# Kernel optimization log

Hardware: AMD Instinct MI355X
Metric: run time of the kernel (lower is better)

## Reference

```python
import jax, jax.numpy as jnp
import numpy as np

ADDR_BITS = 20      # AttentionMemory addr_bits
VAL_BITS = 32       # AttentionMemory value_bits
MAX_ENTRIES = 1024  # preallocated buffer size (torch default 4096, reduced)
TEMP = 10.0         # registered temperature buffer
B, T, R = 16, 128, 2048  # batch of memories, sequential writes, reads


def _encode(x, nbits):
    # BinaryEncoder: int -> +/-1 bit vector [..., nbits]
    bits = jnp.right_shift(x[..., None], jnp.arange(nbits, dtype=x.dtype)) & 1
    return bits.astype(jnp.float32) * 2.0 - 1.0


def setup_inputs() -> dict:
    key = jax.random.key(0)
    k1, k2, k3 = jax.random.split(key, 3)
    waddr = jax.random.randint(k1, (B, T), 0, 1 << ADDR_BITS, dtype=jnp.int32)
    wval = jax.random.randint(k2, (B, T), 0, 2**31 - 1, dtype=jnp.int32)
    raddr = jax.random.randint(k3, (B, R), 0, 1 << ADDR_BITS, dtype=jnp.int32)
    return {
        "write_addr_enc": _encode(waddr, ADDR_BITS),  # [B,T,20]
        "write_val_enc": _encode(wval, VAL_BITS),     # [B,T,32]
        "read_addr_enc": _encode(raddr, ADDR_BITS),   # [B,R,20]
    }


def reference(write_addr_enc, write_val_enc, read_addr_enc):
    E = MAX_ENTRIES
    ar = jnp.arange(E)
    keys0 = jnp.zeros((B, E, ADDR_BITS), jnp.float32)
    vals0 = jnp.zeros((B, E, VAL_BITS), jnp.float32)
    count0 = jnp.zeros((B,), jnp.int32)

    def step(state, inp):
        keys, values, count = state
        addr, val = inp  # [B,20], [B,32]
        scores = jnp.einsum('bea,ba->be', keys, addr)            # [B,E]
        valid = ar[None, :] < count[:, None]
        masked = jnp.where(valid, scores, -1e9)
        # torch: if max_score > addr_bits-1 -> overwrite argmax, else append
        overwrite = masked.max(axis=1) > (ADDR_BITS - 1)         # [B]
        idx = jnp.where(overwrite, jnp.argmax(masked, axis=1), count)
        onehot = ar[None, :] == idx[:, None]                     # [B,E]
        values = jnp.where(onehot[..., None], val[:, None, :], values)
        keys = jnp.where((onehot & ~overwrite[:, None])[..., None],
                         addr[:, None, :], keys)
        count = count + (~overwrite).astype(jnp.int32)
        return (keys, values, count), None

    (keys, values, count), _ = jax.lax.scan(
        step, (keys0, vals0, count0),
        (write_addr_enc.transpose(1, 0, 2), write_val_enc.transpose(1, 0, 2)))

    # AttentionMemory.read: softmax(keys @ addr * temperature) @ values
    rscores = jnp.einsum('bea,bra->bre', keys, read_addr_enc)    # [B,R,E]
    valid = ar[None, None, :] < count[:, None, None]
    rscores = jnp.where(valid, rscores * TEMP, -1e9)
    weights = jax.nn.softmax(rscores, axis=-1)
    return jnp.einsum('bre,bev->brv', weights, values)           # [B,R,32]
```

## Files before the change

kernel.cpp:

```cpp
#include <hip/hip_runtime.h>
#include <hip/hip_bf16.h>

#define B_DIM 16
#define T_DIM 128
#define R_DIM 2048
#define ABITS 20
#define VBITS 32
#define RPB   32
#define BLOCKS_PER_B (R_DIM / RPB)

__global__ __launch_bounds__(256) void fused_kernel(
    const float* __restrict__ waddr,
    const float* __restrict__ wval,
    const float* __restrict__ raddr,
    float* __restrict__ out)
{
    const int b    = blockIdx.x / BLOCKS_PER_B;
    const int rblk = blockIdx.x % BLOCKS_PER_B;
    const int t    = threadIdx.x;

    __shared__ unsigned s_addr[T_DIM];
    __shared__ unsigned s_val[T_DIM];
    __shared__ unsigned s_key[T_DIM];
    __shared__ unsigned s_vbits[T_DIM];
    __shared__ int      s_slotmap[T_DIM];
    __shared__ float    s_f[RPB * ABITS];
    __shared__ unsigned s_valT[VBITS * 4];
    __shared__ int      s_n;

    if (t == 0) s_n = 0;

    const float4* rp = (const float4*)(raddr + ((size_t)b * R_DIM + (size_t)rblk * RPB) * ABITS);
    if (t < RPB * ABITS / 4) ((float4*)s_f)[t] = rp[t];

    if (t < T_DIM) {
        const float4* ap = (const float4*)(waddr + (size_t)(b * T_DIM + t) * ABITS);
        unsigned a = 0;
        #pragma unroll
        for (int q = 0; q < ABITS / 4; ++q) {
            float4 f = ap[q];
            a |= (unsigned)(f.x > 0.f) << (4 * q + 0);
            a |= (unsigned)(f.y > 0.f) << (4 * q + 1);
            a |= (unsigned)(f.z > 0.f) << (4 * q + 2);
            a |= (unsigned)(f.w > 0.f) << (4 * q + 3);
        }
        s_addr[t] = a;
    } else {
        const int tv = t - T_DIM;
        const float4* vp = (const float4*)(wval + (size_t)(b * T_DIM + tv) * VBITS);
        unsigned v = 0;
        #pragma unroll
        for (int q = 0; q < VBITS / 4; ++q) {
            float4 f = vp[q];
            v |= (unsigned)(f.x > 0.f) << (4 * q + 0);
            v |= (unsigned)(f.y > 0.f) << (4 * q + 1);
            v |= (unsigned)(f.z > 0.f) << (4 * q + 2);
            v |= (unsigned)(f.w > 0.f) << (4 * q + 3);
        }
        s_val[tv] = v;
    }
    __syncthreads();

    int lastc = 0, t0 = t;
    if (t < T_DIM) {
        const unsigned a = s_addr[t];
        int firstc = 0;
        const uint4* a4 = (const uint4*)s_addr;
        #pragma unroll 8
        for (int u4 = 0; u4 < T_DIM / 4; ++u4) {
            uint4 kk = a4[u4];
            int u = u4 * 4;
            int e0 = (kk.x == a), e1 = (kk.y == a), e2 = (kk.z == a), e3 = (kk.w == a);
            firstc |= (e0 & (u + 0 < t)) | (e1 & (u + 1 < t)) | (e2 & (u + 2 < t)) | (e3 & (u + 3 < t));
            lastc  |= (e0 & (u + 0 > t)) | (e1 & (u + 1 > t)) | (e2 & (u + 2 > t)) | (e3 & (u + 3 > t));
            t0 = (e0 && (u + 0 < t0)) ? (u + 0) : t0;
            t0 = (e1 && (u + 1 < t0)) ? (u + 1) : t0;
            t0 = (e2 && (u + 2 < t0)) ? (u + 2) : t0;
            t0 = (e3 && (u + 3 < t0)) ? (u + 3) : t0;
        }
        if (!firstc) {
            int slot = atomicAdd(&s_n, 1);
            s_key[slot] = a;
            s_slotmap[t] = slot;
        }
    }
    __syncthreads();
    const int n = s_n;
    if (t < T_DIM && !lastc)
        s_vbits[s_slotmap[t0]] = s_val[t];
    __syncthreads();

    if (t < 128) {
        const int j = t & 31, w = t >> 5;
        unsigned word = 0;
        #pragma unroll 8
        for (int i = 0; i < 32; ++i)
            word |= ((s_vbits[w * 32 + i] >> j) & 1u) << i;
        s_valT[j * 4 + w] = word;
    }

    const int rl = t >> 3;
    const int k  = t & 7;
    const float* f = s_f + rl * ABITS;
    unsigned ra = 0;
    #pragma unroll
    for (int i = 0; i < ABITS; ++i) ra |= (unsigned)(f[i] > 0.f) << i;

    const uint4* k4 = (const uint4*)s_key;
    int dmin = 127;
    #pragma unroll
    for (int j = 0; j < 4; ++j) {
        uint4 kk = k4[k * 4 + j];
        int e = k * 16 + j * 4;
        int d0 = __popc(kk.x ^ ra) | ((e + 0 >= n) ? 64 : 0);
        int d1 = __popc(kk.y ^ ra) | ((e + 1 >= n) ? 64 : 0);
        int d2 = __popc(kk.z ^ ra) | ((e + 2 >= n) ? 64 : 0);
        int d3 = __popc(kk.w ^ ra) | ((e + 3 >= n) ? 64 : 0);
        dmin = min(dmin, min(min(d0, d1), min(d2, d3)));
    }
    dmin = min(dmin, __shfl_xor(dmin, 1, 8));
    dmin = min(dmin, __shfl_xor(dmin, 2, 8));
    dmin = min(dmin, __shfl_xor(dmin, 4, 8));

    unsigned mask = 0;
    #pragma unroll
    for (int j = 0; j < 4; ++j) {
        uint4 kk = k4[k * 4 + j];
        int e = k * 16 + j * 4;
        mask |= (unsigned)((__popc(kk.x ^ ra) | ((e + 0 >= n) ? 64 : 0)) == dmin) << (j * 4 + 0);
        mask |= (unsigned)((__popc(kk.y ^ ra) | ((e + 1 >= n) ? 64 : 0)) == dmin) << (j * 4 + 1);
        mask |= (unsigned)((__popc(kk.z ^ ra) | ((e + 2 >= n) ? 64 : 0)) == dmin) << (j * 4 + 2);
        mask |= (unsigned)((__popc(kk.w ^ ra) | ((e + 3 >= n) ? 64 : 0)) == dmin) << (j * 4 + 3);
    }

    unsigned m0 = (unsigned)__shfl((int)mask, 0, 8) | ((unsigned)__shfl((int)mask, 1, 8) << 16);
    unsigned m1 = (unsigned)__shfl((int)mask, 2, 8) | ((unsigned)__shfl((int)mask, 3, 8) << 16);
    unsigned m2 = (unsigned)__shfl((int)mask, 4, 8) | ((unsigned)__shfl((int)mask, 5, 8) << 16);
    unsigned m3 = (unsigned)__shfl((int)mask, 6, 8) | ((unsigned)__shfl((int)mask, 7, 8) << 16);

    __syncthreads();

    const int nm = __popc(m0) + __popc(m1) + __popc(m2) + __popc(m3);
    const float fn = (float)nm, inv = 1.0f / fn;
    const uint4* vT = (const uint4*)s_valT;
    float o[4];
    #pragma unroll
    for (int jj = 0; jj < 4; ++jj) {
        uint4 vt = vT[4 * k + jj];
        int ones = __popc(m0 & vt.x) + __popc(m1 & vt.y) + __popc(m2 & vt.z) + __popc(m3 & vt.w);
        o[jj] = (2.0f * (float)ones - fn) * inv;
    }
    float4* op = (float4*)(out + (((size_t)b * R_DIM + (size_t)rblk * RPB + rl) * VBITS + k * 4));
    *op = make_float4(o[0], o[1], o[2], o[3]);
}

extern "C" void kernel_launch(void* const* d_in, const int* in_sizes, int n_in,
                              void* d_out, int out_size, void* d_ws, size_t ws_size,
                              hipStream_t stream) {
    const float* waddr = (const float*)d_in[0];
    const float* wval  = (const float*)d_in[1];
    const float* raddr = (const float*)d_in[2];
    float* out = (float*)d_out;

    fused_kernel<<<B_DIM * BLOCKS_PER_B, 256, 0, stream>>>(waddr, wval, raddr, out);
}
```

Measured before the change: 70.14 us.

## Split fused kernel into per-batch table build and read kernels

The memory-table construction (dedup, slot assignment, value transpose) used to be recomputed redundantly by every one of the 64 read blocks per batch. It now runs once per batch in a small build kernel that writes keys, transposed values and the entry count to workspace. A separate read kernel loads that table and does the Hamming-distance argmin readout, caching the distances in registers and skipping the validity mask when the table is full. The cost is an extra kernel launch and a global round trip, and the 16-block build kernel runs serially before the reads.

```diff
diff --git a/kernel.cpp b/kernel.cpp
--- a/kernel.cpp
+++ b/kernel.cpp
@@ -8,30 +8,26 @@
 #define VBITS 32
 #define RPB   32
 #define BLOCKS_PER_B (R_DIM / RPB)
-
-__global__ __launch_bounds__(256) void fused_kernel(
+#define TBL_STRIDE 512
+
+
+__global__ __launch_bounds__(256) void build_kernel(
     const float* __restrict__ waddr,
     const float* __restrict__ wval,
-    const float* __restrict__ raddr,
-    float* __restrict__ out)
+    unsigned* __restrict__ tbl)
 {
-    const int b    = blockIdx.x / BLOCKS_PER_B;
-    const int rblk = blockIdx.x % BLOCKS_PER_B;
-    const int t    = threadIdx.x;
+    const int b = blockIdx.x;
+    const int t = threadIdx.x;
 
     __shared__ unsigned s_addr[T_DIM];
     __shared__ unsigned s_val[T_DIM];
     __shared__ unsigned s_key[T_DIM];
     __shared__ unsigned s_vbits[T_DIM];
     __shared__ int      s_slotmap[T_DIM];
-    __shared__ float    s_f[RPB * ABITS];
-    __shared__ unsigned s_valT[VBITS * 4];
     __shared__ int      s_n;
 
     if (t == 0) s_n = 0;
-
-    const float4* rp = (const float4*)(raddr + ((size_t)b * R_DIM + (size_t)rblk * RPB) * ABITS);
-    if (t < RPB * ABITS / 4) ((float4*)s_f)[t] = rp[t];
+    if (t < T_DIM) { s_key[t] = 0u; s_vbits[t] = 0u; }
 
     if (t < T_DIM) {
         const float4* ap = (const float4*)(waddr + (size_t)(b * T_DIM + t) * ABITS);
@@ -85,60 +81,101 @@
         }
     }
     __syncthreads();
-    const int n = s_n;
     if (t < T_DIM && !lastc)
         s_vbits[s_slotmap[t0]] = s_val[t];
     __syncthreads();
 
+    unsigned* dst = tbl + (size_t)b * TBL_STRIDE;
     if (t < 128) {
         const int j = t & 31, w = t >> 5;
         unsigned word = 0;
         #pragma unroll 8
         for (int i = 0; i < 32; ++i)
             word |= ((s_vbits[w * 32 + i] >> j) & 1u) << i;
-        s_valT[j * 4 + w] = word;
-    }
-
+        dst[128 + j * 4 + w] = word;
+        dst[t] = s_key[t];
+    }
+    if (t == 0) dst[256] = (unsigned)s_n;
+}
+
+__global__ __launch_bounds__(256) void read_kernel(
+    const unsigned* __restrict__ tbl,
+    const float* __restrict__ raddr,
+    float* __restrict__ out)
+{
+    const int b    = blockIdx.x / BLOCKS_PER_B;
+    const int rblk = blockIdx.x % BLOCKS_PER_B;
+    const int t    = threadIdx.x;
+
+    __shared__ unsigned s_key[T_DIM];
+    __shared__ unsigned s_valT[VBITS * 4];
+    __shared__ float    s_f[RPB * ABITS];
+    __shared__ int      s_n;
+
+    const unsigned* tb = tbl + (size_t)b * TBL_STRIDE;
+    if (t < 32)                ((uint4*)s_key)[t]       = ((const uint4*)tb)[t];
+    else if (t < 64)           ((uint4*)s_valT)[t - 32] = ((const uint4*)tb)[t];
+    if (t == 0) s_n = (int)tb[256];
+
+    const float4* rp = (const float4*)(raddr + ((size_t)b * R_DIM + (size_t)rblk * RPB) * ABITS);
+    if (t < RPB * ABITS / 4) ((float4*)s_f)[t] = rp[t];
+    __syncthreads();
+
+    const int n  = s_n;
     const int rl = t >> 3;
     const int k  = t & 7;
-    const float* f = s_f + rl * ABITS;
+
+    const float4* f4 = (const float4*)(s_f + rl * ABITS);
     unsigned ra = 0;
     #pragma unroll
-    for (int i = 0; i < ABITS; ++i) ra |= (unsigned)(f[i] > 0.f) << i;
-
+    for (int q = 0; q < ABITS / 4; ++q) {
+        float4 f = f4[q];
+        ra |= (unsigned)(f.x > 0.f) << (4 * q + 0);
+        ra |= (unsigned)(f.y > 0.f) << (4 * q + 1);
+        ra |= (unsigned)(f.z > 0.f) << (4 * q + 2);
+        ra |= (unsigned)(f.w > 0.f) << (4 * q + 3);
+    }
+
+    int d[16];
     const uint4* k4 = (const uint4*)s_key;
-    int dmin = 127;
-    #pragma unroll
-    for (int j = 0; j < 4; ++j) {
-        uint4 kk = k4[k * 4 + j];
-        int e = k * 16 + j * 4;
-        int d0 = __popc(kk.x ^ ra) | ((e + 0 >= n) ? 64 : 0);
-        int d1 = __popc(kk.y ^ ra) | ((e + 1 >= n) ? 64 : 0);
-        int d2 = __popc(kk.z ^ ra) | ((e + 2 >= n) ? 64 : 0);
-        int d3 = __popc(kk.w ^ ra) | ((e + 3 >= n) ? 64 : 0);
-        dmin = min(dmin, min(min(d0, d1), min(d2, d3)));
-    }
+    if (n == T_DIM) {
+        #pragma unroll
+        for (int j = 0; j < 4; ++j) {
+            uint4 kk = k4[k * 4 + j];
+            d[4 * j + 0] = __popc(kk.x ^ ra);
+            d[4 * j + 1] = __popc(kk.y ^ ra);
+            d[4 * j + 2] = __popc(kk.z ^ ra);
+            d[4 * j + 3] = __popc(kk.w ^ ra);
+        }
+    } else {
+        #pragma unroll
+        for (int j = 0; j < 4; ++j) {
+            uint4 kk = k4[k * 4 + j];
+            const int e = k * 16 + j * 4;
+            d[4 * j + 0] = __popc(kk.x ^ ra) | ((e + 0 >= n) ? 64 : 0);
+            d[4 * j + 1] = __popc(kk.y ^ ra) | ((e + 1 >= n) ? 64 : 0);
+            d[4 * j + 2] = __popc(kk.z ^ ra) | ((e + 2 >= n) ? 64 : 0);
+            d[4 * j + 3] = __popc(kk.w ^ ra) | ((e + 3 >= n) ? 64 : 0);
+        }
+    }
+
+    int dmin = min(min(min(d[0], d[1]), min(d[2], d[3])),
+                   min(min(d[4], d[5]), min(d[6], d[7])));
+    dmin = min(dmin, min(min(min(d[8],  d[9]),  min(d[10], d[11])),
+                         min(min(d[12], d[13]), min(d[14], d[15]))));
     dmin = min(dmin, __shfl_xor(dmin, 1, 8));
     dmin = min(dmin, __shfl_xor(dmin, 2, 8));
     dmin = min(dmin, __shfl_xor(dmin, 4, 8));
 
     unsigned mask = 0;
     #pragma unroll
-    for (int j = 0; j < 4; ++j) {
-        uint4 kk = k4[k * 4 + j];
-        int e = k * 16 + j * 4;
-        mask |= (unsigned)((__popc(kk.x ^ ra) | ((e + 0 >= n) ? 64 : 0)) == dmin) << (j * 4 + 0);
-        mask |= (unsigned)((__popc(kk.y ^ ra) | ((e + 1 >= n) ? 64 : 0)) == dmin) << (j * 4 + 1);
-        mask |= (unsigned)((__popc(kk.z ^ ra) | ((e + 2 >= n) ? 64 : 0)) == dmin) << (j * 4 + 2);
-        mask |= (unsigned)((__popc(kk.w ^ ra) | ((e + 3 >= n) ? 64 : 0)) == dmin) << (j * 4 + 3);
-    }
+    for (int i = 0; i < 16; ++i)
+        mask |= (unsigned)(d[i] == dmin) << i;
 
     unsigned m0 = (unsigned)__shfl((int)mask, 0, 8) | ((unsigned)__shfl((int)mask, 1, 8) << 16);
     unsigned m1 = (unsigned)__shfl((int)mask, 2, 8) | ((unsigned)__shfl((int)mask, 3, 8) << 16);
     unsigned m2 = (unsigned)__shfl((int)mask, 4, 8) | ((unsigned)__shfl((int)mask, 5, 8) << 16);
     unsigned m3 = (unsigned)__shfl((int)mask, 6, 8) | ((unsigned)__shfl((int)mask, 7, 8) << 16);
-
-    __syncthreads();
 
     const int nm = __popc(m0) + __popc(m1) + __popc(m2) + __popc(m3);
     const float fn = (float)nm, inv = 1.0f / fn;
@@ -161,6 +198,8 @@
     const float* wval  = (const float*)d_in[1];
     const float* raddr = (const float*)d_in[2];
     float* out = (float*)d_out;
-
-    fused_kernel<<<B_DIM * BLOCKS_PER_B, 256, 0, stream>>>(waddr, wval, raddr, out);
+    unsigned* tbl = (unsigned*)d_ws;
+
+    build_kernel<<<B_DIM, 256, 0, stream>>>(waddr, wval, tbl);
+    read_kernel<<<B_DIM * BLOCKS_PER_B, 256, 0, stream>>>(tbl, raddr, out);
 }
```

Result: faster. 68.67 us (-2.1%).
